# Kernel tuning notes

Hardware: AMD Instinct MI355X
Metric: run time of the kernel (lower is better)

Reference implementation:

```python
import jax, jax.numpy as jnp
import numpy as np

B, T, H, V, L = 128, 64, 256, 128, 2


def _gru_layer(x_seq, w_ih, w_hh, b_ih, b_hh):
    """PyTorch-convention GRU layer. x_seq: (B,T,Hin) -> (B,T,H), h_last (B,H)."""
    # Precompute input projections once for all timesteps: (B,T,3H)
    xp = jnp.einsum('bti,gi->btg', x_seq, w_ih) + b_ih

    def step(h, xp_t):
        hp = h @ w_hh.T + b_hh                      # (B,3H)
        xr, xz, xn = jnp.split(xp_t, 3, axis=-1)
        hr, hz, hn = jnp.split(hp, 3, axis=-1)
        r = jax.nn.sigmoid(xr + hr)
        z = jax.nn.sigmoid(xz + hz)
        n = jnp.tanh(xn + r * hn)
        h_new = (1.0 - z) * n + z * h
        return h_new, h_new

    h0 = jnp.zeros((x_seq.shape[0], w_hh.shape[1]), x_seq.dtype)
    h_last, ys = jax.lax.scan(step, h0, jnp.swapaxes(xp, 0, 1))  # scan over T
    return jnp.swapaxes(ys, 0, 1), h_last


def setup_inputs() -> dict:
    key = jax.random.key(0)
    ks = jax.random.split(key, 16)
    s = 1.0 / np.sqrt(H)

    def u(k, shape):
        return jax.random.uniform(k, shape, jnp.float32, -s, s)

    x = jax.random.randint(ks[0], (B, T), 0, V)
    embed = jax.random.normal(ks[1], (V, H), jnp.float32) * 0.02
    embed = embed.at[0].set(0.0)  # padding_idx=0
    return {
        'x': x,
        'embed': embed,
        'w_ih0': u(ks[2], (3 * H, H)), 'w_hh0': u(ks[3], (3 * H, H)),
        'b_ih0': u(ks[4], (3 * H,)),   'b_hh0': u(ks[5], (3 * H,)),
        'w_ih1': u(ks[6], (3 * H, H)), 'w_hh1': u(ks[7], (3 * H, H)),
        'b_ih1': u(ks[8], (3 * H,)),   'b_hh1': u(ks[9], (3 * H,)),
        'W_a': u(ks[10], (H, H)),
        'U_a': u(ks[11], (H, H)),
        'v_a': u(ks[12], (H,)),
        'fc_W': u(ks[13], (V, 2 * H)),
        'fc_b': u(ks[14], (V,)),
    }


def reference(x, embed, w_ih0, w_hh0, b_ih0, b_hh0,
              w_ih1, w_hh1, b_ih1, b_hh1,
              W_a, U_a, v_a, fc_W, fc_b):
    # Embedding (dropout is identity in eval-mode reference)
    emb = embed[x]                                   # (B,T,H)
    h1_seq, _ = _gru_layer(emb, w_ih0, w_hh0, b_ih0, b_hh0)
    enc, h_last = _gru_layer(h1_seq, w_ih1, w_hh1, b_ih1, b_hh1)  # (B,T,H)

    # Vectorized per-step Bahdanau attention: queries are enc itself (h_t = enc[:,t])
    Wa_e = enc @ W_a.T                               # (B,T,H) keys, computed once
    Ua_h = enc @ U_a.T                               # (B,T,H) queries
    energy = jnp.einsum('btkh,h->btk',
                        jnp.tanh(Wa_e[:, None, :, :] + Ua_h[:, :, None, :]), v_a)
    alpha = jax.nn.softmax(energy, axis=-1)          # (B,T,T)
    ctx = jnp.einsum('btk,bkh->bth', alpha, enc)     # (B,T,H)

    combined = jnp.concatenate([enc, ctx], axis=-1)  # (B,T,2H)
    logits = combined @ fc_W.T + fc_b                # (B,T,V)
    return logits, h_last
```

## Files before the change

kernel.cpp:

```cpp
#include <hip/hip_runtime.h>
#include <math.h>

#define BB 128
#define TT 64
#define HH 256
#define G3 768
#define VV 128

typedef _Float16 half8 __attribute__((ext_vector_type(8)));
typedef float f32x4 __attribute__((ext_vector_type(4)));

__global__ __launch_bounds__(256) void pack_whh_f16(const float* __restrict__ w,
                                                    _Float16* __restrict__ out) {
    int d = blockIdx.x * 256 + threadIdx.x;
    int e   = d & 7;
    int l   = (d >> 3) & 63;
    int kap = (d >> 9) & 7;
    int wt  = d >> 12;
    int wv  = wt / 6, tau = wt % 6;
    int ncol = (tau >> 1) * 256 + wv * 32 + (tau & 1) * 16 + (l & 15);
    int k    = kap * 32 + (l >> 4) * 8 + e;
    out[d] = (_Float16)w[ncol * HH + k];
}

__global__ __launch_bounds__(256) void prep_bias(const float* __restrict__ b_ih,
                                                 const float* __restrict__ b_hh,
                                                 float* __restrict__ outb) {
    int j = blockIdx.x * 256 + threadIdx.x;
    outb[j] = b_ih[j] + (j < 2 * HH ? b_hh[j] : 0.f);
}

__global__ __launch_bounds__(256) void gemm_bt(
    const float* __restrict__ A1, int lda1, int K1,
    const float* __restrict__ A2, int lda2, int K2,
    const float* __restrict__ Bw, int ldb,
    const float* __restrict__ bias,
    float* __restrict__ C, int ldc, int M, int N, int permmode)
{
    __shared__ alignas(16) float As[16][68];
    __shared__ alignas(16) float Bs[16][68];
    const int tid = threadIdx.x;
    const int lc = tid & 15, lr = tid >> 4;
    const int ty = tid >> 4, tx = tid & 15;
    const int row0 = blockIdx.y * 64, col0 = blockIdx.x * 64;
    float acc[4][4] = {};
    const int KT = K1 + K2;

    for (int k0 = 0; k0 < KT; k0 += 16) {
        const float* Ap; int lda, kk0;
        if (k0 < K1) { Ap = A1; lda = lda1; kk0 = k0; }
        else         { Ap = A2; lda = lda2; kk0 = k0 - K1; }
#pragma unroll
        for (int r = 0; r < 4; ++r) {
            As[lc][lr + 16 * r] = Ap[(row0 + lr + 16 * r) * lda + kk0 + lc];
            Bs[lc][lr + 16 * r] = Bw[(col0 + lr + 16 * r) * ldb + k0 + lc];
        }
        __syncthreads();
#pragma unroll
        for (int kk = 0; kk < 16; ++kk) {
            const float4 a4 = *(const float4*)&As[kk][ty * 4];
            const float4 b4 = *(const float4*)&Bs[kk][tx * 4];
            const float av[4] = {a4.x, a4.y, a4.z, a4.w};
            const float bv[4] = {b4.x, b4.y, b4.z, b4.w};
#pragma unroll
            for (int i = 0; i < 4; ++i)
#pragma unroll
                for (int j = 0; j < 4; ++j)
                    acc[i][j] += av[i] * bv[j];
        }
        __syncthreads();
    }

    float bv[4];
#pragma unroll
    for (int j = 0; j < 4; ++j)
        bv[j] = bias ? bias[col0 + tx * 4 + j] : 0.f;
#pragma unroll
    for (int i = 0; i < 4; ++i) {
        const int r = row0 + ty * 4 + i;
        if (permmode == 0) {
            float4 o;
            o.x = acc[i][0] + bv[0];
            o.y = acc[i][1] + bv[1];
            o.z = acc[i][2] + bv[2];
            o.w = acc[i][3] + bv[3];
            *(float4*)&C[r * ldc + col0 + tx * 4] = o;
        } else {
            const int orow = (permmode == 2) ? ((r & 63) * BB + (r >> 6)) : r;
#pragma unroll
            for (int jj = 0; jj < 4; ++jj) {
                const int j = col0 + tx * 4 + jj;
                const int g = j >> 8, c = j & 255;
                C[orow * 1024 + c * 4 + g] = acc[i][jj] + bv[jj];
            }
        }
    }
}

__global__ __launch_bounds__(512, 2) void gru_mfma(
    const _Float16* __restrict__ wp,
    const float* __restrict__ b_hh,
    const float* __restrict__ xsrc,
    const int*   __restrict__ xidx,
    float* __restrict__ out_seq,
    float* __restrict__ hlast,
    int mode)
{
    __shared__ alignas(16) _Float16 hbuf[2][16][264];
    __shared__ int tok[16][TT];
    const int tid = threadIdx.x;
    const int wv = tid >> 6, l = tid & 63;
    const int l15 = l & 15, lhi = l >> 4;
    const int r0 = blockIdx.x * 16;

    for (int i = tid; i < 16 * 264; i += 512) ((_Float16*)hbuf[0])[i] = (_Float16)0.f;
    if (mode == 0) {
        ((int*)tok)[tid]       = xidx[r0 * TT + tid];
        ((int*)tok)[tid + 512] = xidx[r0 * TT + tid + 512];
    }

    half8 W[48];
    const half8* wp8 = (const half8*)wp;
    const int fb = wv * 48 * 64;
#pragma unroll
    for (int f = 0; f < 48; ++f) W[f] = wp8[fb + f * 64 + l];

    const int colbase = wv * 32 + l15;
    const float bhn0 = b_hh[2 * HH + colbase];
    const float bhn1 = b_hh[2 * HH + colbase + 16];
    __syncthreads();

    int cur = 0;
    for (int t = 0; t < TT; ++t) {
        float2 xrz[2][4]; float xn[2][4];
#pragma unroll
        for (int s = 0; s < 2; ++s) {
            const int c = colbase + 16 * s;
#pragma unroll
            for (int reg = 0; reg < 4; ++reg) {
                const int rr = lhi * 4 + reg;
                const long row = (mode == 0) ? (long)tok[rr][t]
                                             : (long)t * BB + (r0 + rr);
                const float* p = &xsrc[row * 1024 + c * 4];
                xrz[s][reg] = *(const float2*)p;
                xn[s][reg]  = p[2];
            }
        }

        f32x4 acc[6];
#pragma unroll
        for (int tau = 0; tau < 6; ++tau) acc[tau] = (f32x4)0.f;

#pragma unroll
        for (int kap = 0; kap < 8; ++kap) {
            const half8 a = *(const half8*)&hbuf[cur][l15][kap * 32 + lhi * 8];
#pragma unroll
            for (int tau = 0; tau < 6; ++tau)
                acc[tau] = __builtin_amdgcn_mfma_f32_16x16x32_f16(
                    a, W[tau * 8 + kap], acc[tau], 0, 0, 0);
        }

#pragma unroll
        for (int s = 0; s < 2; ++s) {
            const int col = colbase + s * 16;
            const float bhn = s ? bhn1 : bhn0;
#pragma unroll
            for (int reg = 0; reg < 4; ++reg) {
                const int row = lhi * 4 + reg;
                const float ho = (float)hbuf[cur][row][col];
                const float pr = acc[0 + s][reg] + xrz[s][reg].x;
                const float pz = acc[2 + s][reg] + xrz[s][reg].y;
                const float hn = acc[4 + s][reg] + bhn;
                const float rg = 1.f / (1.f + __expf(-pr));
                const float zg = 1.f / (1.f + __expf(-pz));
                const float npre = xn[s][reg] + rg * hn;
                const float e2 = __expf(2.f * npre);
                const float ng = (e2 - 1.f) / (e2 + 1.f);
                const float hnew = (1.f - zg) * ng + zg * ho;
                hbuf[cur ^ 1][row][col] = (_Float16)hnew;
                out_seq[((r0 + row) * TT + t) * HH + col] = hnew;
            }
        }

        cur ^= 1;
        asm volatile("s_waitcnt lgkmcnt(0)" ::: "memory");
        __builtin_amdgcn_s_barrier();
        asm volatile("" ::: "memory");
    }

    if (mode == 1) {
#pragma unroll
        for (int s = 0; s < 2; ++s) {
            const int col = colbase + s * 16;
#pragma unroll
            for (int reg = 0; reg < 4; ++reg) {
                const int row = lhi * 4 + reg;
                hlast[(r0 + row) * HH + col] = (float)hbuf[cur][row][col];
            }
        }
    }
}

__device__ __forceinline__ float tanh_fast(float x) {
    const float e = __expf(2.f * x);
    return (e - 1.f) / (e + 1.f);
}

__global__ __launch_bounds__(256) void attn_kernel(
    const float* __restrict__ WU,
    const float* __restrict__ enc,
    const float* __restrict__ v_a,
    float* __restrict__ ctx)
{
    __shared__ float q[HH], va[HH], sm[TT];
    const int tid = threadIdx.x;
    const int t = blockIdx.x, b = blockIdx.y;

    q[tid]  = WU[(b * TT + t) * 512 + 256 + tid];
    va[tid] = v_a[tid];
    __syncthreads();

    const int w = tid >> 6, lane = tid & 63;
#pragma unroll 4
    for (int i = 0; i < 16; ++i) {
        const int k = w * 16 + i;
        const float* we = WU + (b * TT + k) * 512;
        float s = 0.f;
#pragma unroll
        for (int c = 0; c < 4; ++c) {
            const int h = lane + 64 * c;
            s += va[h] * tanh_fast(we[h] + q[h]);
        }
#pragma unroll
        for (int off = 32; off > 0; off >>= 1) s += __shfl_xor(s, off);
        if (lane == 0) sm[k] = s;
    }
    __syncthreads();

    if (tid < TT) {
        const float e = sm[tid];
        float mx = e;
#pragma unroll
        for (int off = 32; off > 0; off >>= 1) mx = fmaxf(mx, __shfl_xor(mx, off));
        const float p = __expf(e - mx);
        float sum = p;
#pragma unroll
        for (int off = 32; off > 0; off >>= 1) sum += __shfl_xor(sum, off);
        sm[tid] = p / sum;
    }
    __syncthreads();

    float c = 0.f;
    for (int k = 0; k < TT; ++k)
        c += sm[k] * enc[(b * TT + k) * HH + tid];
    ctx[(b * TT + t) * HH + tid] = c;
}

extern "C" void kernel_launch(void* const* d_in, const int* in_sizes, int n_in,
                              void* d_out, int out_size, void* d_ws, size_t ws_size,
                              hipStream_t stream) {
    const int*   x     = (const int*)  d_in[0];
    const float* embed = (const float*)d_in[1];
    const float* w_ih0 = (const float*)d_in[2];
    const float* w_hh0 = (const float*)d_in[3];
    const float* b_ih0 = (const float*)d_in[4];
    const float* b_hh0 = (const float*)d_in[5];
    const float* w_ih1 = (const float*)d_in[6];
    const float* w_hh1 = (const float*)d_in[7];
    const float* b_ih1 = (const float*)d_in[8];
    const float* b_hh1 = (const float*)d_in[9];
    const float* W_a   = (const float*)d_in[10];
    const float* U_a   = (const float*)d_in[11];
    const float* v_a   = (const float*)d_in[12];
    const float* fc_W  = (const float*)d_in[13];
    const float* fc_b  = (const float*)d_in[14];
    float* out = (float*)d_out;

    float* ws = (float*)d_ws;
    _Float16* wT0 = (_Float16*)ws;
    _Float16* wT1 = wT0 + 196608;
    float* bias0 = ws    + 196608;
    float* bias1 = bias0 + 768;
    float* P0    = bias1 + 768;
    float* h1    = P0    + 131072;
    float* enc   = h1    + 2097152;
    float* WU_B  = enc   + 2097152;
    float* xp1   = WU_B  + 131072;
    float* WU    = xp1;
    float* ctxb  = xp1   + 4194304;

    float* logits = out;
    float* hlast  = out + BB * TT * VV;

    pack_whh_f16<<<768, 256, 0, stream>>>(w_hh0, wT0);
    pack_whh_f16<<<768, 256, 0, stream>>>(w_hh1, wT1);
    prep_bias<<<3, 256, 0, stream>>>(b_ih0, b_hh0, bias0);
    prep_bias<<<3, 256, 0, stream>>>(b_ih1, b_hh1, bias1);
    hipMemcpyAsync(WU_B, W_a, HH * HH * sizeof(float),
                   hipMemcpyDeviceToDevice, stream);
    hipMemcpyAsync(WU_B + HH * HH, U_a, HH * HH * sizeof(float),
                   hipMemcpyDeviceToDevice, stream);

    gemm_bt<<<dim3(G3 / 64, VV / 64), 256, 0, stream>>>(
        embed, HH, HH, nullptr, 0, 0, w_ih0, HH, bias0, P0, 0, VV, G3, 1);

    gru_mfma<<<BB / 16, 512, 0, stream>>>(wT0, b_hh0, P0, x, h1, nullptr, 0);

    gemm_bt<<<dim3(G3 / 64, BB * TT / 64), 256, 0, stream>>>(
        h1, HH, HH, nullptr, 0, 0, w_ih1, HH, bias1, xp1, 0, BB * TT, G3, 2);

    gru_mfma<<<BB / 16, 512, 0, stream>>>(wT1, b_hh1, xp1, nullptr, enc, hlast, 1);

    gemm_bt<<<dim3(512 / 64, BB * TT / 64), 256, 0, stream>>>(
        enc, HH, HH, nullptr, 0, 0, WU_B, HH, nullptr, WU, 512, BB * TT, 512, 0);

    attn_kernel<<<dim3(TT, BB), 256, 0, stream>>>(WU, enc, v_a, ctxb);

    gemm_bt<<<dim3(VV / 64, BB * TT / 64), 256, 0, stream>>>(
        enc, HH, HH, ctxb, HH, HH, fc_W, 2 * HH, fc_b, logits, VV, BB * TT, VV, 0);
}
```

Baseline: 723.9 us.

## Prefetch GRU input projections into LDS asynchronously one step ahead

The GRU recurrence kernel now prefetches the next timestep's input-projection rows into a double-buffered shared-memory array using global_load_lds, so those global loads overlap the current step's MFMA and gate math instead of sitting on the serial critical path. The projection GEMMs write a plain row-major 768-wide layout with float4 stores, replacing the interleaved gate layout with scalar scattered stores. The cost is about 99KB of extra LDS per block and a barrier with a partial vmcnt wait, whose count must match the number of outstanding loads per step.

```diff
diff --git a/kernel.cpp b/kernel.cpp
--- a/kernel.cpp
+++ b/kernel.cpp
@@ -78,22 +78,13 @@
 #pragma unroll
     for (int i = 0; i < 4; ++i) {
         const int r = row0 + ty * 4 + i;
-        if (permmode == 0) {
-            float4 o;
-            o.x = acc[i][0] + bv[0];
-            o.y = acc[i][1] + bv[1];
-            o.z = acc[i][2] + bv[2];
-            o.w = acc[i][3] + bv[3];
-            *(float4*)&C[r * ldc + col0 + tx * 4] = o;
-        } else {
-            const int orow = (permmode == 2) ? ((r & 63) * BB + (r >> 6)) : r;
-#pragma unroll
-            for (int jj = 0; jj < 4; ++jj) {
-                const int j = col0 + tx * 4 + jj;
-                const int g = j >> 8, c = j & 255;
-                C[orow * 1024 + c * 4 + g] = acc[i][jj] + bv[jj];
-            }
-        }
+        const int orow = (permmode == 2) ? ((r & 63) * BB + (r >> 6)) : r;
+        float4 o;
+        o.x = acc[i][0] + bv[0];
+        o.y = acc[i][1] + bv[1];
+        o.z = acc[i][2] + bv[2];
+        o.w = acc[i][3] + bv[3];
+        *(float4*)&C[orow * ldc + col0 + tx * 4] = o;
     }
 }
 
@@ -107,6 +98,7 @@
     int mode)
 {
     __shared__ alignas(16) _Float16 hbuf[2][16][264];
+    __shared__ alignas(16) float xbuf[2][16][776];
     __shared__ int tok[16][TT];
     const int tid = threadIdx.x;
     const int wv = tid >> 6, l = tid & 63;
@@ -130,22 +122,29 @@
     const float bhn1 = b_hh[2 * HH + colbase + 16];
     __syncthreads();
 
+    auto stage = [&](int buf, int t) {
+#pragma unroll
+        for (int rr = 0; rr < 2; ++rr) {
+            const int row = wv * 2 + rr;
+            const float* rb = (mode == 0)
+                ? xsrc + (long)tok[row][t] * G3
+                : xsrc + ((long)t * BB + r0 + row) * G3;
+#pragma unroll
+            for (int c = 0; c < 3; ++c) {
+                __builtin_amdgcn_global_load_lds(
+                    (const __attribute__((address_space(1))) unsigned int*)(rb + c * 256 + l * 4),
+                    (__attribute__((address_space(3))) unsigned int*)&xbuf[buf][row][c * 256],
+                    16, 0, 0);
+            }
+        }
+    };
+
+    stage(0, 0);
+    asm volatile("s_waitcnt vmcnt(0) lgkmcnt(0)\n\ts_barrier" ::: "memory");
+
     int cur = 0;
     for (int t = 0; t < TT; ++t) {
-        float2 xrz[2][4]; float xn[2][4];
-#pragma unroll
-        for (int s = 0; s < 2; ++s) {
-            const int c = colbase + 16 * s;
-#pragma unroll
-            for (int reg = 0; reg < 4; ++reg) {
-                const int rr = lhi * 4 + reg;
-                const long row = (mode == 0) ? (long)tok[rr][t]
-                                             : (long)t * BB + (r0 + rr);
-                const float* p = &xsrc[row * 1024 + c * 4];
-                xrz[s][reg] = *(const float2*)p;
-                xn[s][reg]  = p[2];
-            }
-        }
+        if (t + 1 < TT) stage(cur ^ 1, t + 1);
 
         f32x4 acc[6];
 #pragma unroll
@@ -167,13 +166,16 @@
 #pragma unroll
             for (int reg = 0; reg < 4; ++reg) {
                 const int row = lhi * 4 + reg;
+                const float xr = xbuf[cur][row][col];
+                const float xz = xbuf[cur][row][col + HH];
+                const float xnv = xbuf[cur][row][col + 2 * HH];
                 const float ho = (float)hbuf[cur][row][col];
-                const float pr = acc[0 + s][reg] + xrz[s][reg].x;
-                const float pz = acc[2 + s][reg] + xrz[s][reg].y;
+                const float pr = acc[0 + s][reg] + xr;
+                const float pz = acc[2 + s][reg] + xz;
                 const float hn = acc[4 + s][reg] + bhn;
                 const float rg = 1.f / (1.f + __expf(-pr));
                 const float zg = 1.f / (1.f + __expf(-pz));
-                const float npre = xn[s][reg] + rg * hn;
+                const float npre = xnv + rg * hn;
                 const float e2 = __expf(2.f * npre);
                 const float ng = (e2 - 1.f) / (e2 + 1.f);
                 const float hnew = (1.f - zg) * ng + zg * ho;
@@ -183,9 +185,7 @@
         }
 
         cur ^= 1;
-        asm volatile("s_waitcnt lgkmcnt(0)" ::: "memory");
-        __builtin_amdgcn_s_barrier();
-        asm volatile("" ::: "memory");
+        asm volatile("s_waitcnt vmcnt(8) lgkmcnt(0)\n\ts_barrier" ::: "memory");
     }
 
     if (mode == 1) {
@@ -282,7 +282,7 @@
     float* bias0 = ws    + 196608;
     float* bias1 = bias0 + 768;
     float* P0    = bias1 + 768;
-    float* h1    = P0    + 131072;
+    float* h1    = P0    + 98304;
     float* enc   = h1    + 2097152;
     float* WU_B  = enc   + 2097152;
     float* xp1   = WU_B  + 131072;
@@ -302,12 +302,12 @@
                    hipMemcpyDeviceToDevice, stream);
 
     gemm_bt<<<dim3(G3 / 64, VV / 64), 256, 0, stream>>>(
-        embed, HH, HH, nullptr, 0, 0, w_ih0, HH, bias0, P0, 0, VV, G3, 1);
+        embed, HH, HH, nullptr, 0, 0, w_ih0, HH, bias0, P0, G3, VV, G3, 0);
 
     gru_mfma<<<BB / 16, 512, 0, stream>>>(wT0, b_hh0, P0, x, h1, nullptr, 0);
 
     gemm_bt<<<dim3(G3 / 64, BB * TT / 64), 256, 0, stream>>>(
-        h1, HH, HH, nullptr, 0, 0, w_ih1, HH, bias1, xp1, 0, BB * TT, G3, 2);
+        h1, HH, HH, nullptr, 0, 0, w_ih1, HH, bias1, xp1, G3, BB * TT, G3, 2);
 
     gru_mfma<<<BB / 16, 512, 0, stream>>>(wT1, b_hh1, xp1, nullptr, enc, hlast, 1);
 
```

New measurement: 724.2 us. Within noise of the previous version (+0.0%).
